# Performance work log

Hardware: AMD Instinct MI355X
Metric: run time of the kernel (lower is better)

## Reference

```python
import jax, jax.numpy as jnp
import numpy as np

HEAD_SIZE = 64
N_EMBD = 768

def setup_inputs() -> dict:
    key = jax.random.key(0)
    kx, kq, kk, kv = jax.random.split(key, 4)
    x = jax.random.normal(kx, (4, 4096, N_EMBD), dtype=jnp.float32)
    s = 1.0 / np.sqrt(N_EMBD)
    Wq = jax.random.normal(kq, (N_EMBD, HEAD_SIZE), dtype=jnp.float32) * s
    Wk = jax.random.normal(kk, (N_EMBD, HEAD_SIZE), dtype=jnp.float32) * s
    Wv = jax.random.normal(kv, (N_EMBD, HEAD_SIZE), dtype=jnp.float32) * s
    return {"x": x, "Wq": Wq, "Wk": Wk, "Wv": Wv}

def reference(x, Wq, Wk, Wv):
    b, t, c = x.shape
    h = Wq.shape[1]
    q = jnp.einsum('btc,ch->bth', x, Wq)
    k = jnp.einsum('btc,ch->bth', x, Wk)
    v = jnp.einsum('btc,ch->bth', x, Wv)
    scores = jnp.einsum('bqh,bkh->bqk', q, k) / jnp.sqrt(jnp.float32(h))
    causal = jnp.tril(jnp.ones((t, t), dtype=bool))  # [t,t]
    scores = jnp.where(causal, scores, -jnp.inf)
    attn = jax.nn.softmax(scores, axis=-1)
    return jnp.einsum('bqk,bkh->bqh', attn, v)
```

## Files before the change

### kernel.cpp

```cpp
#include <hip/hip_runtime.h>
#include <math.h>

#define BB 4
#define TT 4096
#define CC 768
#define HH 64
#define NN 192
#define LDP 72
#define GR 32
#define XSTR 776
#define SC2 0.180336880f

typedef __bf16 bf16x8 __attribute__((ext_vector_type(8)));
typedef float floatx4 __attribute__((ext_vector_type(4)));
typedef float floatx16 __attribute__((ext_vector_type(16)));
typedef unsigned short u16x8 __attribute__((ext_vector_type(8)));

__device__ inline unsigned short f2bf(float f) {
    union { __bf16 b; unsigned short u; } v;
    v.b = (__bf16)f;
    return v.u;
}
__device__ inline float bf2f(unsigned short u) {
    union { unsigned int u; float f; } v;
    v.u = (unsigned int)u << 16;
    return v.f;
}
__device__ inline unsigned cvtpk(float lo, float hi) {
    unsigned d;
    asm("v_cvt_pk_bf16_f32 %0, %1, %2" : "=v"(d) : "v"(lo), "v"(hi));
    return d;
}

__global__ __launch_bounds__(256) void wprep(const float* __restrict__ Wq,
                                             const float* __restrict__ Wk,
                                             const float* __restrict__ Wv,
                                             unsigned short* __restrict__ wtf) {
    const int idx = blockIdx.x * 256 + threadIdx.x;
    if (idx >= NN * CC) return;
    const int j = idx & 7;
    const int lane = (idx >> 3) & 63;
    const int rest = idx >> 9;
    const int kg = rest % 24;
    const int n_tile = rest / 24;
    const int c = kg * 32 + (lane >> 4) * 8 + j;
    const int n = n_tile * 16 + (lane & 15);
    const float* W = (n < 64) ? Wq : (n < 128) ? Wk : Wv;
    wtf[idx] = f2bf(W[c * HH + (n & 63)]);
}

__global__ __launch_bounds__(256) void qkv_gemm(const float* __restrict__ x,
                                                const unsigned short* __restrict__ wtf,
                                                unsigned short* __restrict__ qb,
                                                unsigned short* __restrict__ kb,
                                                unsigned short* __restrict__ vbt) {
    __shared__ unsigned short As[GR * XSTR];

    const int tid = threadIdx.x;
    const int w = tid >> 6, lane = tid & 63;
    const int l15 = lane & 15, quad = lane >> 4;
    const int m0 = blockIdx.x * GR;
    const int n0 = w * 48;
    const int nt0 = w * 3;

    const float* xbase = x + (size_t)m0 * CC;
#pragma unroll
    for (int e = 0; e < 12; ++e) {
        const int c = tid + 256 * e;
        const int r = c / 96, off = (c - r * 96) * 8;
        const float4 v0 = *(const float4*)(xbase + (size_t)c * 8);
        const float4 v1 = *(const float4*)(xbase + (size_t)c * 8 + 4);
        u16x8 pk;
        pk[0] = f2bf(v0.x); pk[1] = f2bf(v0.y); pk[2] = f2bf(v0.z); pk[3] = f2bf(v0.w);
        pk[4] = f2bf(v1.x); pk[5] = f2bf(v1.y); pk[6] = f2bf(v1.z); pk[7] = f2bf(v1.w);
        *(u16x8*)(As + r * XSTR + off) = pk;
    }
    __syncthreads();

    floatx4 acc[2][3] = {};
#pragma unroll 4
    for (int step = 0; step < 12; ++step) {
        bf16x8 a0[2], a1[2];
#pragma unroll
        for (int rg = 0; rg < 2; ++rg) {
            const unsigned short* ap = As + (16 * rg + l15) * XSTR + step * 64 + quad * 8;
            a0[rg] = *(const bf16x8*)(ap);
            a1[rg] = *(const bf16x8*)(ap + 32);
        }
#pragma unroll
        for (int j = 0; j < 3; ++j) {
            const unsigned short* bp =
                wtf + ((size_t)((nt0 + j) * 24 + 2 * step) * 64 + lane) * 8;
            const bf16x8 b0 = *(const bf16x8*)(bp);
            const bf16x8 b1 = *(const bf16x8*)(bp + 512);
#pragma unroll
            for (int rg = 0; rg < 2; ++rg) {
                acc[rg][j] = __builtin_amdgcn_mfma_f32_16x16x32_bf16(a0[rg], b0, acc[rg][j], 0, 0, 0);
                acc[rg][j] = __builtin_amdgcn_mfma_f32_16x16x32_bf16(a1[rg], b1, acc[rg][j], 0, 0, 0);
            }
        }
    }

    const int b = m0 >> 12;
#pragma unroll
    for (int j = 0; j < 3; ++j) {
        const int n = n0 + j * 16 + l15;
        const int mid = n >> 6;
        const int h = n & 63;
#pragma unroll
        for (int rg = 0; rg < 2; ++rg) {
            const int tloc = (m0 & (TT - 1)) + 16 * rg + quad * 4;
            if (mid == 2) {
                ushort4 pk;
                pk.x = f2bf(acc[rg][j][0]); pk.y = f2bf(acc[rg][j][1]);
                pk.z = f2bf(acc[rg][j][2]); pk.w = f2bf(acc[rg][j][3]);
                *(ushort4*)(vbt + ((size_t)b * HH + h) * TT + tloc) = pk;
            } else {
                unsigned short* dst = (mid == 0) ? qb : kb;
#pragma unroll
                for (int r = 0; r < 4; ++r)
                    dst[(size_t)(m0 + 16 * rg + quad * 4 + r) * HH + h] = f2bf(acc[rg][j][r]);
            }
        }
    }
}

template<int CH>
__global__ __launch_bounds__(256) void attn_part(const unsigned short* __restrict__ qb,
                                                 const unsigned short* __restrict__ kb,
                                                 const unsigned short* __restrict__ vbt,
                                                 unsigned short* __restrict__ Opart,
                                                 float* __restrict__ lsum,
                                                 float* __restrict__ out) {
    __shared__ __align__(16) unsigned char smem[16896];
    unsigned short* Ks  = (unsigned short*)smem;
    unsigned short* VTs = (unsigned short*)(smem + 8192);
    float (*Osh)[2][16][64] = (float(*)[2][16][64])smem;
    float* Lsh = (float*)(smem + 16384);

    constexpr int NG = 64 / CH;
    constexpr int TOTB = CH * (NG * (NG + 1)) / 2;

    const int b = blockIdx.x & 3;
    int rem = TOTB - 1 - (blockIdx.x >> 2);
    int g = 0;
    while (rem >= CH * (g + 1)) { rem -= CH * (g + 1); ++g; }
    const int qt = g * CH + rem / (g + 1);
    const int ch = rem - (rem / (g + 1)) * (g + 1);

    const int q0  = qt * 64;
    const int tid = threadIdx.x;
    const int w = tid >> 6, lane = tid & 63;
    const int wq = w >> 1, wk = w & 1;
    const int l31 = lane & 31, hi = lane >> 5;

    const unsigned short* Qb  = qb  + (size_t)b * TT * HH;
    const unsigned short* Kb  = kb  + (size_t)b * TT * HH;
    const unsigned short* VTb = vbt + (size_t)b * HH * TT;

    bf16x8 qf[4];
    {
        const unsigned short* qp = Qb + (size_t)(q0 + 32 * wq + l31) * HH + 8 * hi;
#pragma unroll
        for (int s = 0; s < 4; ++s) qf[s] = *(const bf16x8*)(qp + 16 * s);
    }

    floatx16 o0 = {}, o1 = {};
    float lacc = 0.f;

    const int kt0 = ch * CH;
    const int kt1 = min(kt0 + CH, qt + 1);

    const int sr = tid >> 3;
    const int slot = tid & 7;
    const int swz = ((slot ^ (sr & 7)) << 3);

    const int kr = 32 * wk + l31;
    const int krow_off = kr * 64;
    const int ksw = (kr & 7);
    const int vd0 = l31, vd1 = 32 + l31;

    u16x8 nk0, nk1, nv0, nv1;
    {
        const unsigned short* Kt = Kb + (size_t)(kt0 * 64) * HH;
        const unsigned short* Vt = VTb + kt0 * 64;
        nk0 = *(const u16x8*)(Kt + (size_t)sr * HH + slot * 8);
        nk1 = *(const u16x8*)(Kt + (size_t)(sr + 32) * HH + slot * 8);
        nv0 = *(const u16x8*)(Vt + (size_t)sr * TT + slot * 8);
        nv1 = *(const u16x8*)(Vt + (size_t)(sr + 32) * TT + slot * 8);
    }

    for (int kt = kt0; kt < kt1; ++kt) {
        __syncthreads();
        *(u16x8*)(Ks  + sr * 64 + swz)        = nk0;
        *(u16x8*)(Ks  + (sr + 32) * 64 + swz) = nk1;
        *(u16x8*)(VTs + sr * 64 + swz)        = nv0;
        *(u16x8*)(VTs + (sr + 32) * 64 + swz) = nv1;
        __syncthreads();

        if (kt + 1 < kt1) {
            const unsigned short* Kt = Kb + (size_t)((kt + 1) * 64) * HH;
            const unsigned short* Vt = VTb + (kt + 1) * 64;
            nk0 = *(const u16x8*)(Kt + (size_t)sr * HH + slot * 8);
            nk1 = *(const u16x8*)(Kt + (size_t)(sr + 32) * HH + slot * 8);
            nv0 = *(const u16x8*)(Vt + (size_t)sr * TT + slot * 8);
            nv1 = *(const u16x8*)(Vt + (size_t)(sr + 32) * TT + slot * 8);
        }

        bf16x8 kc[4];
#pragma unroll
        for (int s = 0; s < 4; ++s) {
            const int sl = 2 * s + hi;
            kc[s] = *(const bf16x8*)(Ks + krow_off + ((sl ^ ksw) << 3));
        }
        bf16x8 vv[4];
#pragma unroll
        for (int i = 0; i < 4; ++i) {
            const int db = i >> 1, m = i & 1;
            const int d = db ? vd1 : vd0;
            const int sl = 4 * wk + 2 * m + hi;
            vv[i] = *(const bf16x8*)(VTs + d * 64 + ((sl ^ (d & 7)) << 3));
        }

        floatx16 sa = {};
#pragma unroll
        for (int s = 0; s < 4; ++s)
            sa = __builtin_amdgcn_mfma_f32_32x32x16_bf16(kc[s], qf[s], sa, 0, 0, 0);

        float st[16];
#pragma unroll
        for (int r = 0; r < 16; ++r) st[r] = sa[r] * SC2;

        if (kt == qt) {
            const int qloc = 32 * wq + l31;
#pragma unroll
            for (int r = 0; r < 16; ++r) {
                const int kloc = 32 * wk + (r & 3) + 8 * (r >> 2) + 4 * hi;
                if (kloc > qloc) st[r] = -INFINITY;
            }
        }

#pragma unroll
        for (int r = 0; r < 16; ++r) {
            const float p = exp2f(st[r]);
            st[r] = p;
            lacc += p;
        }

        bf16x8 pf[2];
#pragma unroll
        for (int m = 0; m < 2; ++m) {
            const unsigned d0 = cvtpk(st[8 * m + 0], st[8 * m + 1]);
            const unsigned d1 = cvtpk(st[8 * m + 2], st[8 * m + 3]);
            const unsigned d2 = cvtpk(st[8 * m + 4], st[8 * m + 5]);
            const unsigned d3 = cvtpk(st[8 * m + 6], st[8 * m + 7]);
            const unsigned e0 = (unsigned)__shfl_xor((int)d0, 32);
            const unsigned e1 = (unsigned)__shfl_xor((int)d1, 32);
            const unsigned e2 = (unsigned)__shfl_xor((int)d2, 32);
            const unsigned e3 = (unsigned)__shfl_xor((int)d3, 32);
            union { unsigned u[4]; bf16x8 v; } pk;
            pk.u[0] = hi ? e2 : d0;
            pk.u[1] = hi ? e3 : d1;
            pk.u[2] = hi ? d2 : e0;
            pk.u[3] = hi ? d3 : e1;
            pf[m] = pk.v;
        }

        o0 = __builtin_amdgcn_mfma_f32_32x32x16_bf16(vv[0], pf[0], o0, 0, 0, 0);
        o0 = __builtin_amdgcn_mfma_f32_32x32x16_bf16(vv[1], pf[1], o0, 0, 0, 0);
        o1 = __builtin_amdgcn_mfma_f32_32x32x16_bf16(vv[2], pf[0], o1, 0, 0, 0);
        o1 = __builtin_amdgcn_mfma_f32_32x32x16_bf16(vv[3], pf[1], o1, 0, 0, 0);
    }

    __syncthreads();
    if (wk == 1) {
#pragma unroll
        for (int r = 0; r < 16; ++r) {
            Osh[wq][0][r][lane] = o0[r];
            Osh[wq][1][r][lane] = o1[r];
        }
        Lsh[wq * 64 + lane] = lacc;
    }
    __syncthreads();
    if (wk == 1) return;
#pragma unroll
    for (int r = 0; r < 16; ++r) {
        o0[r] += Osh[wq][0][r][lane];
        o1[r] += Osh[wq][1][r][lane];
    }
    lacc += Lsh[wq * 64 + lane];
    const float l = lacc + __shfl_xor(lacc, 32);

    if (qt < CH) {
        float* outp = out + ((size_t)b * TT + q0 + 32 * wq + l31) * HH;
        const float inv = 1.f / l;
#pragma unroll
        for (int r = 0; r < 16; ++r) {
            const int dd = (r & 3) + 8 * (r >> 2) + 4 * hi;
            outp[dd]      = o0[r] * inv;
            outp[32 + dd] = o1[r] * inv;
        }
        return;
    }

    const int pbase = ((b * 64 + qt) * NG + ch) * 64;
    unsigned short* Op = Opart + ((size_t)pbase + 32 * wq + l31) * HH;
#pragma unroll
    for (int a = 0; a < 4; ++a) {
        *(unsigned*)(Op + 8 * a + 4 * hi)          = cvtpk(o0[4 * a + 0], o0[4 * a + 1]);
        *(unsigned*)(Op + 8 * a + 4 * hi + 2)      = cvtpk(o0[4 * a + 2], o0[4 * a + 3]);
        *(unsigned*)(Op + 32 + 8 * a + 4 * hi)     = cvtpk(o1[4 * a + 0], o1[4 * a + 1]);
        *(unsigned*)(Op + 32 + 8 * a + 4 * hi + 2) = cvtpk(o1[4 * a + 2], o1[4 * a + 3]);
    }
    if (hi == 0) lsum[pbase + 32 * wq + l31] = l;
}

template<int CH>
__global__ __launch_bounds__(256) void attn_merge(const unsigned short* __restrict__ Opart,
                                                  const float* __restrict__ lsum,
                                                  float* __restrict__ out) {
    constexpr int NG = 64 / CH;
    const int g = blockIdx.x * 256 + threadIdx.x;
    const int row = g >> 3, oct = g & 7;
    const int b = row >> 12, t = row & (TT - 1);
    const int qt = t >> 6, rloc = t & 63;
    if (qt < CH) return;
    const int nchunk = qt / CH + 1;
    const int pbase = ((b * 64 + qt) * NG) * 64 + rloc;
    const int d0 = oct * 8;

    float L = 0.f;
    float a[8] = {};
    for (int c = 0; c < nchunk; ++c) {
        const int idx = pbase + c * 64;
        L += lsum[idx];
        const u16x8 pv = *(const u16x8*)(Opart + (size_t)idx * HH + d0);
#pragma unroll
        for (int k = 0; k < 8; ++k) a[k] += bf2f(pv[k]);
    }
    const float inv = 1.f / L;
    float4 o0, o1;
    o0.x = a[0] * inv; o0.y = a[1] * inv; o0.z = a[2] * inv; o0.w = a[3] * inv;
    o1.x = a[4] * inv; o1.y = a[5] * inv; o1.z = a[6] * inv; o1.w = a[7] * inv;
    float* dst = out + (size_t)row * HH + d0;
    *(float4*)(dst) = o0;
    *(float4*)(dst + 4) = o1;
}

__global__ __launch_bounds__(256) void attn_full(const unsigned short* __restrict__ qb,
                                                 const unsigned short* __restrict__ kb,
                                                 const unsigned short* __restrict__ vbt,
                                                 float* __restrict__ out) {
    __shared__ unsigned short Ks[64 * LDP];
    __shared__ unsigned short VTs[64 * LDP];
    __shared__ unsigned short Ps[4][16 * LDP];

    const int b   = blockIdx.x >> 6;
    const int qt  = blockIdx.x & 63;
    const int q0  = qt * 64;
    const int tid = threadIdx.x;
    const int w = tid >> 6, lane = tid & 63;
    const int l15 = lane & 15, quad = lane >> 4;

    const unsigned short* Qb  = qb  + (size_t)b * TT * HH;
    const unsigned short* Kb  = kb  + (size_t)b * TT * HH;
    const unsigned short* VTb = vbt + (size_t)b * HH * TT;

    const int qrow = q0 + 16 * w + l15;
    const bf16x8 qf0 = *(const bf16x8*)(Qb + (size_t)qrow * HH + quad * 8);
    const bf16x8 qf1 = *(const bf16x8*)(Qb + (size_t)qrow * HH + 32 + quad * 8);

    floatx4 O[4] = {};
    floatx4 lacc = {0.f, 0.f, 0.f, 0.f};

    for (int kt = 0; kt <= qt; ++kt) {
        __syncthreads();
        const unsigned short* Kt = Kb + (size_t)(kt * 64) * HH;
        const unsigned short* Vt = VTb + kt * 64;
#pragma unroll
        for (int e = 0; e < 2; ++e) {
            const int chunk = tid + 256 * e;
            const int r = chunk >> 3, c0 = (chunk & 7) * 8;
            *(u16x8*)(Ks + r * LDP + c0)  = *(const u16x8*)(Kt + r * HH + c0);
            *(u16x8*)(VTs + r * LDP + c0) = *(const u16x8*)(Vt + (size_t)r * TT + c0);
        }
        __syncthreads();

        floatx4 s[4];
#pragma unroll
        for (int ki = 0; ki < 4; ++ki) {
            const bf16x8 kf0 = *(const bf16x8*)(Ks + (16 * ki + l15) * LDP + quad * 8);
            const bf16x8 kf1 = *(const bf16x8*)(Ks + (16 * ki + l15) * LDP + 32 + quad * 8);
            floatx4 c = {};
            c = __builtin_amdgcn_mfma_f32_16x16x32_bf16(qf0, kf0, c, 0, 0, 0);
            c = __builtin_amdgcn_mfma_f32_16x16x32_bf16(qf1, kf1, c, 0, 0, 0);
            s[ki] = c * SC2;
        }
        if (kt == qt) {
#pragma unroll
            for (int ki = 0; ki < 4; ++ki)
#pragma unroll
                for (int r = 0; r < 4; ++r)
                    if (16 * ki + l15 > 16 * w + quad * 4 + r) s[ki][r] = -INFINITY;
        }
#pragma unroll
        for (int ki = 0; ki < 4; ++ki)
#pragma unroll
            for (int r = 0; r < 4; ++r) {
                const float p = exp2f(s[ki][r]);
                s[ki][r] = p; lacc[r] += p;
            }

        unsigned short* Pw = Ps[w];
#pragma unroll
        for (int ki = 0; ki < 4; ++ki)
#pragma unroll
            for (int r = 0; r < 4; ++r)
                Pw[(quad * 4 + r) * LDP + 16 * ki + l15] = f2bf(s[ki][r]);

        const bf16x8 pf0 = *(const bf16x8*)(Pw + l15 * LDP + quad * 8);
        const bf16x8 pf1 = *(const bf16x8*)(Pw + l15 * LDP + 32 + quad * 8);
#pragma unroll
        for (int di = 0; di < 4; ++di) {
            const bf16x8 vf0 = *(const bf16x8*)(VTs + (16 * di + l15) * LDP + quad * 8);
            const bf16x8 vf1 = *(const bf16x8*)(VTs + (16 * di + l15) * LDP + 32 + quad * 8);
            O[di] = __builtin_amdgcn_mfma_f32_16x16x32_bf16(pf0, vf0, O[di], 0, 0, 0);
            O[di] = __builtin_amdgcn_mfma_f32_16x16x32_bf16(pf1, vf1, O[di], 0, 0, 0);
        }
    }
    float l_r[4];
#pragma unroll
    for (int r = 0; r < 4; ++r) {
        float v = lacc[r];
#pragma unroll
        for (int msk = 8; msk >= 1; msk >>= 1) v += __shfl_xor(v, msk, 64);
        l_r[r] = v;
    }
    float* outp = out + ((size_t)b * TT + q0 + 16 * w) * HH;
#pragma unroll
    for (int di = 0; di < 4; ++di)
#pragma unroll
        for (int r = 0; r < 4; ++r)
            outp[(quad * 4 + r) * HH + 16 * di + l15] = O[di][r] / l_r[r];
}

extern "C" void kernel_launch(void* const* d_in, const int* in_sizes, int n_in,
                              void* d_out, int out_size, void* d_ws, size_t ws_size,
                              hipStream_t stream) {
    const float* x  = (const float*)d_in[0];
    const float* Wq = (const float*)d_in[1];
    const float* Wk = (const float*)d_in[2];
    const float* Wv = (const float*)d_in[3];
    float* out = (float*)d_out;

    const size_t nQKV = (size_t)BB * TT * HH;
    unsigned short* qb  = (unsigned short*)d_ws;
    unsigned short* kb  = qb + nQKV;
    unsigned short* vbt = kb + nQKV;
    unsigned short* wtf = vbt + nQKV;
    unsigned short* Opart = wtf + (size_t)NN * CC;

    const size_t prows8  = (size_t)BB * 64 * 8 * 64;
    const size_t prows16 = (size_t)BB * 64 * 4 * 64;
    float* lsum8  = (float*)(Opart + prows8 * HH);
    float* lsum16 = (float*)(Opart + prows16 * HH);
    const size_t need8  = (size_t)((char*)(lsum8  + prows8)  - (char*)d_ws);
    const size_t need16 = (size_t)((char*)(lsum16 + prows16) - (char*)d_ws);

    wprep<<<(NN * CC + 255) / 256, 256, 0, stream>>>(Wq, Wk, Wv, wtf);
    qkv_gemm<<<(BB * TT) / GR, 256, 0, stream>>>(x, wtf, qb, kb, vbt);
    if (ws_size >= need8) {
        attn_part<8><<<BB * 288, 256, 0, stream>>>(qb, kb, vbt, Opart, lsum8, out);
        attn_merge<8><<<(BB * TT * 8) / 256, 256, 0, stream>>>(Opart, lsum8, out);
    } else if (ws_size >= need16) {
        attn_part<16><<<BB * 160, 256, 0, stream>>>(qb, kb, vbt, Opart, lsum16, out);
        attn_merge<16><<<(BB * TT * 8) / 256, 256, 0, stream>>>(Opart, lsum16, out);
    } else {
        attn_full<<<BB * (TT / 64), 256, 0, stream>>>(qb, kb, vbt, out);
    }
}
```

Baseline: 128.3 us.

## Double-buffer K/V tiles in LDS to drop one barrier per iteration

Splits the shared-memory K and V^T staging into two ping-pong buffers. The next tile is written into the idle buffer while the current one is consumed, and global prefetch now runs two tiles ahead. This removes the second __syncthreads per key tile and lets the LDS stores overlap with the MFMA work. In exchange, shared memory per block roughly doubles, which may reduce how many blocks fit per CU.

```diff
diff --git a/kernel.cpp b/kernel.cpp
--- a/kernel.cpp
+++ b/kernel.cpp
@@ -132,11 +132,9 @@
                                                  unsigned short* __restrict__ Opart,
                                                  float* __restrict__ lsum,
                                                  float* __restrict__ out) {
-    __shared__ __align__(16) unsigned char smem[16896];
-    unsigned short* Ks  = (unsigned short*)smem;
-    unsigned short* VTs = (unsigned short*)(smem + 8192);
+    __shared__ __align__(16) unsigned short smem[16384];
     float (*Osh)[2][16][64] = (float(*)[2][16][64])smem;
-    float* Lsh = (float*)(smem + 16384);
+    float* Lsh = (float*)(smem + 8192);
 
     constexpr int NG = 64 / CH;
     constexpr int TOTB = CH * (NG * (NG + 1)) / 2;
@@ -189,29 +187,52 @@
         nv0 = *(const u16x8*)(Vt + (size_t)sr * TT + slot * 8);
         nv1 = *(const u16x8*)(Vt + (size_t)(sr + 32) * TT + slot * 8);
     }
+    {
+        unsigned short* Ks0  = smem;
+        unsigned short* VTs0 = smem + 4096;
+        *(u16x8*)(Ks0  + sr * 64 + swz)        = nk0;
+        *(u16x8*)(Ks0  + (sr + 32) * 64 + swz) = nk1;
+        *(u16x8*)(VTs0 + sr * 64 + swz)        = nv0;
+        *(u16x8*)(VTs0 + (sr + 32) * 64 + swz) = nv1;
+    }
+    if (kt0 + 1 < kt1) {
+        const unsigned short* Kt = Kb + (size_t)((kt0 + 1) * 64) * HH;
+        const unsigned short* Vt = VTb + (kt0 + 1) * 64;
+        nk0 = *(const u16x8*)(Kt + (size_t)sr * HH + slot * 8);
+        nk1 = *(const u16x8*)(Kt + (size_t)(sr + 32) * HH + slot * 8);
+        nv0 = *(const u16x8*)(Vt + (size_t)sr * TT + slot * 8);
+        nv1 = *(const u16x8*)(Vt + (size_t)(sr + 32) * TT + slot * 8);
+    }
 
     for (int kt = kt0; kt < kt1; ++kt) {
+        const int p = (kt - kt0) & 1;
         __syncthreads();
-        *(u16x8*)(Ks  + sr * 64 + swz)        = nk0;
-        *(u16x8*)(Ks  + (sr + 32) * 64 + swz) = nk1;
-        *(u16x8*)(VTs + sr * 64 + swz)        = nv0;
-        *(u16x8*)(VTs + (sr + 32) * 64 + swz) = nv1;
-        __syncthreads();
 
         if (kt + 1 < kt1) {
-            const unsigned short* Kt = Kb + (size_t)((kt + 1) * 64) * HH;
-            const unsigned short* Vt = VTb + (kt + 1) * 64;
-            nk0 = *(const u16x8*)(Kt + (size_t)sr * HH + slot * 8);
-            nk1 = *(const u16x8*)(Kt + (size_t)(sr + 32) * HH + slot * 8);
-            nv0 = *(const u16x8*)(Vt + (size_t)sr * TT + slot * 8);
-            nv1 = *(const u16x8*)(Vt + (size_t)(sr + 32) * TT + slot * 8);
-        }
+            unsigned short* Ksn  = smem + (p ^ 1) * 8192;
+            unsigned short* VTsn = Ksn + 4096;
+            *(u16x8*)(Ksn  + sr * 64 + swz)        = nk0;
+            *(u16x8*)(Ksn  + (sr + 32) * 64 + swz) = nk1;
+            *(u16x8*)(VTsn + sr * 64 + swz)        = nv0;
+            *(u16x8*)(VTsn + (sr + 32) * 64 + swz) = nv1;
+            if (kt + 2 < kt1) {
+                const unsigned short* Kt = Kb + (size_t)((kt + 2) * 64) * HH;
+                const unsigned short* Vt = VTb + (kt + 2) * 64;
+                nk0 = *(const u16x8*)(Kt + (size_t)sr * HH + slot * 8);
+                nk1 = *(const u16x8*)(Kt + (size_t)(sr + 32) * HH + slot * 8);
+                nv0 = *(const u16x8*)(Vt + (size_t)sr * TT + slot * 8);
+                nv1 = *(const u16x8*)(Vt + (size_t)(sr + 32) * TT + slot * 8);
+            }
+        }
+
+        const unsigned short* Ksc  = smem + p * 8192;
+        const unsigned short* VTsc = Ksc + 4096;
 
         bf16x8 kc[4];
 #pragma unroll
         for (int s = 0; s < 4; ++s) {
             const int sl = 2 * s + hi;
-            kc[s] = *(const bf16x8*)(Ks + krow_off + ((sl ^ ksw) << 3));
+            kc[s] = *(const bf16x8*)(Ksc + krow_off + ((sl ^ ksw) << 3));
         }
         bf16x8 vv[4];
 #pragma unroll
@@ -219,7 +240,7 @@
             const int db = i >> 1, m = i & 1;
             const int d = db ? vd1 : vd0;
             const int sl = 4 * wk + 2 * m + hi;
-            vv[i] = *(const bf16x8*)(VTs + d * 64 + ((sl ^ (d & 7)) << 3));
+            vv[i] = *(const bf16x8*)(VTsc + d * 64 + ((sl ^ (d & 7)) << 3));
         }
 
         floatx16 sa = {};
@@ -242,9 +263,9 @@
 
 #pragma unroll
         for (int r = 0; r < 16; ++r) {
-            const float p = exp2f(st[r]);
-            st[r] = p;
-            lacc += p;
+            const float p2 = exp2f(st[r]);
+            st[r] = p2;
+            lacc += p2;
         }
 
         bf16x8 pf[2];
```

Result: no change. 130.3 us (+1.5%).

## Fuse partial-attention merge into attn_part via last-block atomic counter

Applied to the files above, without the earlier changes.

Removes the separate attn_merge kernel. Each attn_part block now bumps a per-(batch, q-tile) atomic counter after writing its partial output and row sum. The last block to arrive for a tile reads all partials and writes the normalised output. The counters are zeroed inside wprep, which saves a kernel launch and a pass over the grid, but the last-arriving blocks now carry the merge work serially, which may lengthen the tail. The no-workspace fallback passes wprep an int alias of wtf as the counter buffer, so its zeroing can race with the wtf writes.

```diff
diff --git a/kernel.cpp b/kernel.cpp
--- a/kernel.cpp
+++ b/kernel.cpp
@@ -35,8 +35,10 @@
 __global__ __launch_bounds__(256) void wprep(const float* __restrict__ Wq,
                                              const float* __restrict__ Wk,
                                              const float* __restrict__ Wv,
-                                             unsigned short* __restrict__ wtf) {
+                                             unsigned short* __restrict__ wtf,
+                                             int* __restrict__ cnt) {
     const int idx = blockIdx.x * 256 + threadIdx.x;
+    if (idx < 256) cnt[idx] = 0;
     if (idx >= NN * CC) return;
     const int j = idx & 7;
     const int lane = (idx >> 3) & 63;
@@ -131,12 +133,14 @@
                                                  const unsigned short* __restrict__ vbt,
                                                  unsigned short* __restrict__ Opart,
                                                  float* __restrict__ lsum,
+                                                 int* __restrict__ cnt,
                                                  float* __restrict__ out) {
-    __shared__ __align__(16) unsigned char smem[16896];
+    __shared__ __align__(16) unsigned char smem[16912];
     unsigned short* Ks  = (unsigned short*)smem;
     unsigned short* VTs = (unsigned short*)(smem + 8192);
     float (*Osh)[2][16][64] = (float(*)[2][16][64])smem;
     float* Lsh = (float*)(smem + 16384);
+    int* flag  = (int*)(smem + 16896);
 
     constexpr int NG = 64 / CH;
     constexpr int TOTB = CH * (NG * (NG + 1)) / 2;
@@ -282,69 +286,76 @@
         Lsh[wq * 64 + lane] = lacc;
     }
     __syncthreads();
-    if (wk == 1) return;
-#pragma unroll
-    for (int r = 0; r < 16; ++r) {
-        o0[r] += Osh[wq][0][r][lane];
-        o1[r] += Osh[wq][1][r][lane];
-    }
-    lacc += Lsh[wq * 64 + lane];
+    if (wk == 0) {
+#pragma unroll
+        for (int r = 0; r < 16; ++r) {
+            o0[r] += Osh[wq][0][r][lane];
+            o1[r] += Osh[wq][1][r][lane];
+        }
+        lacc += Lsh[wq * 64 + lane];
+    }
     const float l = lacc + __shfl_xor(lacc, 32);
 
     if (qt < CH) {
-        float* outp = out + ((size_t)b * TT + q0 + 32 * wq + l31) * HH;
-        const float inv = 1.f / l;
-#pragma unroll
-        for (int r = 0; r < 16; ++r) {
-            const int dd = (r & 3) + 8 * (r >> 2) + 4 * hi;
-            outp[dd]      = o0[r] * inv;
-            outp[32 + dd] = o1[r] * inv;
+        if (wk == 0) {
+            float* outp = out + ((size_t)b * TT + q0 + 32 * wq + l31) * HH;
+            const float inv = 1.f / l;
+#pragma unroll
+            for (int r = 0; r < 16; ++r) {
+                const int dd = (r & 3) + 8 * (r >> 2) + 4 * hi;
+                outp[dd]      = o0[r] * inv;
+                outp[32 + dd] = o1[r] * inv;
+            }
         }
         return;
     }
 
     const int pbase = ((b * 64 + qt) * NG + ch) * 64;
-    unsigned short* Op = Opart + ((size_t)pbase + 32 * wq + l31) * HH;
-#pragma unroll
-    for (int a = 0; a < 4; ++a) {
-        *(unsigned*)(Op + 8 * a + 4 * hi)          = cvtpk(o0[4 * a + 0], o0[4 * a + 1]);
-        *(unsigned*)(Op + 8 * a + 4 * hi + 2)      = cvtpk(o0[4 * a + 2], o0[4 * a + 3]);
-        *(unsigned*)(Op + 32 + 8 * a + 4 * hi)     = cvtpk(o1[4 * a + 0], o1[4 * a + 1]);
-        *(unsigned*)(Op + 32 + 8 * a + 4 * hi + 2) = cvtpk(o1[4 * a + 2], o1[4 * a + 3]);
-    }
-    if (hi == 0) lsum[pbase + 32 * wq + l31] = l;
-}
-
-template<int CH>
-__global__ __launch_bounds__(256) void attn_merge(const unsigned short* __restrict__ Opart,
-                                                  const float* __restrict__ lsum,
-                                                  float* __restrict__ out) {
-    constexpr int NG = 64 / CH;
-    const int g = blockIdx.x * 256 + threadIdx.x;
-    const int row = g >> 3, oct = g & 7;
-    const int b = row >> 12, t = row & (TT - 1);
-    const int qt = t >> 6, rloc = t & 63;
-    if (qt < CH) return;
+    if (wk == 0) {
+        unsigned short* Op = Opart + ((size_t)pbase + 32 * wq + l31) * HH;
+#pragma unroll
+        for (int a = 0; a < 4; ++a) {
+            *(unsigned*)(Op + 8 * a + 4 * hi)          = cvtpk(o0[4 * a + 0], o0[4 * a + 1]);
+            *(unsigned*)(Op + 8 * a + 4 * hi + 2)      = cvtpk(o0[4 * a + 2], o0[4 * a + 3]);
+            *(unsigned*)(Op + 32 + 8 * a + 4 * hi)     = cvtpk(o1[4 * a + 0], o1[4 * a + 1]);
+            *(unsigned*)(Op + 32 + 8 * a + 4 * hi + 2) = cvtpk(o1[4 * a + 2], o1[4 * a + 3]);
+        }
+        if (hi == 0) lsum[pbase + 32 * wq + l31] = l;
+    }
+
     const int nchunk = qt / CH + 1;
-    const int pbase = ((b * 64 + qt) * NG) * 64 + rloc;
-    const int d0 = oct * 8;
-
-    float L = 0.f;
-    float a[8] = {};
-    for (int c = 0; c < nchunk; ++c) {
-        const int idx = pbase + c * 64;
-        L += lsum[idx];
-        const u16x8 pv = *(const u16x8*)(Opart + (size_t)idx * HH + d0);
-#pragma unroll
-        for (int k = 0; k < 8; ++k) a[k] += bf2f(pv[k]);
-    }
-    const float inv = 1.f / L;
-    float4 o0, o1;
-    o0.x = a[0] * inv; o0.y = a[1] * inv; o0.z = a[2] * inv; o0.w = a[3] * inv;
-    o1.x = a[4] * inv; o1.y = a[5] * inv; o1.z = a[6] * inv; o1.w = a[7] * inv;
-    float* dst = out + (size_t)row * HH + d0;
-    *(float4*)(dst) = o0;
-    *(float4*)(dst + 4) = o1;
+    __syncthreads();
+    if (tid == 0) {
+        __threadfence();
+        const int old = atomicAdd(&cnt[b * 64 + qt], 1);
+        *flag = (old == nchunk - 1);
+    }
+    __syncthreads();
+    if (!*flag) return;
+    __threadfence();
+
+    const int gbase = (b * 64 + qt) * NG * 64;
+    const int oct = tid & 7, d0m = oct * 8;
+#pragma unroll
+    for (int pass = 0; pass < 2; ++pass) {
+        const int rr = (tid >> 3) + 32 * pass;
+        float L = 0.f;
+        float a[8] = {};
+        for (int c = 0; c < nchunk; ++c) {
+            const int idx = gbase + c * 64 + rr;
+            L += lsum[idx];
+            const u16x8 pv = *(const u16x8*)(Opart + (size_t)idx * HH + d0m);
+#pragma unroll
+            for (int k = 0; k < 8; ++k) a[k] += bf2f(pv[k]);
+        }
+        const float inv = 1.f / L;
+        float4 v0, v1;
+        v0.x = a[0] * inv; v0.y = a[1] * inv; v0.z = a[2] * inv; v0.w = a[3] * inv;
+        v1.x = a[4] * inv; v1.y = a[5] * inv; v1.z = a[6] * inv; v1.w = a[7] * inv;
+        float* dst = out + ((size_t)b * TT + q0 + rr) * HH + d0m;
+        *(float4*)(dst) = v0;
+        *(float4*)(dst + 4) = v1;
+    }
 }
 
 __global__ __launch_bounds__(256) void attn_full(const unsigned short* __restrict__ qb,
@@ -464,18 +475,22 @@
     const size_t prows16 = (size_t)BB * 64 * 4 * 64;
     float* lsum8  = (float*)(Opart + prows8 * HH);
     float* lsum16 = (float*)(Opart + prows16 * HH);
-    const size_t need8  = (size_t)((char*)(lsum8  + prows8)  - (char*)d_ws);
-    const size_t need16 = (size_t)((char*)(lsum16 + prows16) - (char*)d_ws);
-
-    wprep<<<(NN * CC + 255) / 256, 256, 0, stream>>>(Wq, Wk, Wv, wtf);
-    qkv_gemm<<<(BB * TT) / GR, 256, 0, stream>>>(x, wtf, qb, kb, vbt);
+    int* cnt8  = (int*)(lsum8 + prows8);
+    int* cnt16 = (int*)(lsum16 + prows16);
+    const size_t need8  = (size_t)((char*)(cnt8  + 256) - (char*)d_ws);
+    const size_t need16 = (size_t)((char*)(cnt16 + 256) - (char*)d_ws);
+
     if (ws_size >= need8) {
-        attn_part<8><<<BB * 288, 256, 0, stream>>>(qb, kb, vbt, Opart, lsum8, out);
-        attn_merge<8><<<(BB * TT * 8) / 256, 256, 0, stream>>>(Opart, lsum8, out);
+        wprep<<<(NN * CC + 255) / 256, 256, 0, stream>>>(Wq, Wk, Wv, wtf, cnt8);
+        qkv_gemm<<<(BB * TT) / GR, 256, 0, stream>>>(x, wtf, qb, kb, vbt);
+        attn_part<8><<<BB * 288, 256, 0, stream>>>(qb, kb, vbt, Opart, lsum8, cnt8, out);
     } else if (ws_size >= need16) {
-        attn_part<16><<<BB * 160, 256, 0, stream>>>(qb, kb, vbt, Opart, lsum16, out);
-        attn_merge<16><<<(BB * TT * 8) / 256, 256, 0, stream>>>(Opart, lsum16, out);
+        wprep<<<(NN * CC + 255) / 256, 256, 0, stream>>>(Wq, Wk, Wv, wtf, cnt16);
+        qkv_gemm<<<(BB * TT) / GR, 256, 0, stream>>>(x, wtf, qb, kb, vbt);
+        attn_part<16><<<BB * 160, 256, 0, stream>>>(qb, kb, vbt, Opart, lsum16, cnt16, out);
     } else {
+        wprep<<<(NN * CC + 255) / 256, 256, 0, stream>>>(Wq, Wk, Wv, wtf, (int*)wtf);
+        qkv_gemm<<<(BB * TT) / GR, 256, 0, stream>>>(x, wtf, qb, kb, vbt);
         attn_full<<<BB * (TT / 64), 256, 0, stream>>>(qb, kb, vbt, out);
     }
 }
```

Result: slower. 221.7 us (+72.7%).

## Use 128-row query tiles with each wave owning 32 queries over full key tile

Applied to the files above, without the earlier changes.

The split-KV attention kernel now gives each block 128 query rows, one 32-row slice per wave, and each wave walks both 32-key halves of every 64-key tile. Before, waves split the keys and combined their partial outputs through shared memory. The new layout removes that cross-wave reduction and its extra barriers, and each K/V tile loaded into shared memory now serves twice as many queries. It also skips 32-key sub-blocks that lie fully above the causal diagonal. In exchange the grid has half as many blocks, and the partial-output buffer layout and the merge kernel are re-indexed to match.

```diff
diff --git a/kernel.cpp b/kernel.cpp
--- a/kernel.cpp
+++ b/kernel.cpp
@@ -132,27 +132,26 @@
                                                  unsigned short* __restrict__ Opart,
                                                  float* __restrict__ lsum,
                                                  float* __restrict__ out) {
-    __shared__ __align__(16) unsigned char smem[16896];
-    unsigned short* Ks  = (unsigned short*)smem;
-    unsigned short* VTs = (unsigned short*)(smem + 8192);
-    float (*Osh)[2][16][64] = (float(*)[2][16][64])smem;
-    float* Lsh = (float*)(smem + 16384);
-
-    constexpr int NG = 64 / CH;
-    constexpr int TOTB = CH * (NG * (NG + 1)) / 2;
+    __shared__ __align__(16) unsigned short Ks[64 * 64];
+    __shared__ __align__(16) unsigned short VTs[64 * 64];
+
+    constexpr int W  = CH / 2;
+    constexpr int NB = 32 / W;
+    constexpr int NG = NB;
+    constexpr int TOTB = W * NB * (NB + 1) / 2;
 
     const int b = blockIdx.x & 3;
     int rem = TOTB - 1 - (blockIdx.x >> 2);
     int g = 0;
-    while (rem >= CH * (g + 1)) { rem -= CH * (g + 1); ++g; }
-    const int qt = g * CH + rem / (g + 1);
+    while (rem >= W * (g + 1)) { rem -= W * (g + 1); ++g; }
+    const int qt = g * W + rem / (g + 1);
     const int ch = rem - (rem / (g + 1)) * (g + 1);
 
-    const int q0  = qt * 64;
+    const int q0  = qt * 128;
     const int tid = threadIdx.x;
     const int w = tid >> 6, lane = tid & 63;
-    const int wq = w >> 1, wk = w & 1;
     const int l31 = lane & 31, hi = lane >> 5;
+    const int qbase = q0 + 32 * w;
 
     const unsigned short* Qb  = qb  + (size_t)b * TT * HH;
     const unsigned short* Kb  = kb  + (size_t)b * TT * HH;
@@ -160,7 +159,7 @@
 
     bf16x8 qf[4];
     {
-        const unsigned short* qp = Qb + (size_t)(q0 + 32 * wq + l31) * HH + 8 * hi;
+        const unsigned short* qp = Qb + (size_t)(qbase + l31) * HH + 8 * hi;
 #pragma unroll
         for (int s = 0; s < 4; ++s) qf[s] = *(const bf16x8*)(qp + 16 * s);
     }
@@ -168,16 +167,16 @@
     floatx16 o0 = {}, o1 = {};
     float lacc = 0.f;
 
+    const int nkt = 2 * qt + 2;
     const int kt0 = ch * CH;
-    const int kt1 = min(kt0 + CH, qt + 1);
+    const int kt1 = min(kt0 + CH, nkt);
 
     const int sr = tid >> 3;
     const int slot = tid & 7;
     const int swz = ((slot ^ (sr & 7)) << 3);
 
-    const int kr = 32 * wk + l31;
-    const int krow_off = kr * 64;
-    const int ksw = (kr & 7);
+    const int krow_off0 = l31 * 64;
+    const int ksw = (l31 & 7);
     const int vd0 = l31, vd1 = 32 + l31;
 
     u16x8 nk0, nk1, nv0, nv1;
@@ -207,92 +206,81 @@
             nv1 = *(const u16x8*)(Vt + (size_t)(sr + 32) * TT + slot * 8);
         }
 
-        bf16x8 kc[4];
-#pragma unroll
-        for (int s = 0; s < 4; ++s) {
-            const int sl = 2 * s + hi;
-            kc[s] = *(const bf16x8*)(Ks + krow_off + ((sl ^ ksw) << 3));
-        }
-        bf16x8 vv[4];
-#pragma unroll
-        for (int i = 0; i < 4; ++i) {
-            const int db = i >> 1, m = i & 1;
-            const int d = db ? vd1 : vd0;
-            const int sl = 4 * wk + 2 * m + hi;
-            vv[i] = *(const bf16x8*)(VTs + d * 64 + ((sl ^ (d & 7)) << 3));
-        }
-
-        floatx16 sa = {};
-#pragma unroll
-        for (int s = 0; s < 4; ++s)
-            sa = __builtin_amdgcn_mfma_f32_32x32x16_bf16(kc[s], qf[s], sa, 0, 0, 0);
-
-        float st[16];
-#pragma unroll
-        for (int r = 0; r < 16; ++r) st[r] = sa[r] * SC2;
-
-        if (kt == qt) {
-            const int qloc = 32 * wq + l31;
+#pragma unroll
+        for (int ks = 0; ks < 2; ++ks) {
+            const int kb32 = kt * 64 + 32 * ks;
+            if (kb32 > qbase + 31) continue;
+
+            bf16x8 kc[4];
+#pragma unroll
+            for (int s = 0; s < 4; ++s) {
+                const int sl = 2 * s + hi;
+                kc[s] = *(const bf16x8*)(Ks + 32 * 64 * ks + krow_off0 + ((sl ^ ksw) << 3));
+            }
+
+            floatx16 sa = {};
+#pragma unroll
+            for (int s = 0; s < 4; ++s)
+                sa = __builtin_amdgcn_mfma_f32_32x32x16_bf16(kc[s], qf[s], sa, 0, 0, 0);
+
+            float st[16];
+#pragma unroll
+            for (int r = 0; r < 16; ++r) st[r] = sa[r] * SC2;
+
+            if (kb32 == qbase) {
+#pragma unroll
+                for (int r = 0; r < 16; ++r) {
+                    const int key = (r & 3) + 8 * (r >> 2) + 4 * hi;
+                    if (key > l31) st[r] = -INFINITY;
+                }
+            }
+
 #pragma unroll
             for (int r = 0; r < 16; ++r) {
-                const int kloc = 32 * wk + (r & 3) + 8 * (r >> 2) + 4 * hi;
-                if (kloc > qloc) st[r] = -INFINITY;
-            }
-        }
-
-#pragma unroll
-        for (int r = 0; r < 16; ++r) {
-            const float p = exp2f(st[r]);
-            st[r] = p;
-            lacc += p;
-        }
-
-        bf16x8 pf[2];
-#pragma unroll
-        for (int m = 0; m < 2; ++m) {
-            const unsigned d0 = cvtpk(st[8 * m + 0], st[8 * m + 1]);
-            const unsigned d1 = cvtpk(st[8 * m + 2], st[8 * m + 3]);
-            const unsigned d2 = cvtpk(st[8 * m + 4], st[8 * m + 5]);
-            const unsigned d3 = cvtpk(st[8 * m + 6], st[8 * m + 7]);
-            const unsigned e0 = (unsigned)__shfl_xor((int)d0, 32);
-            const unsigned e1 = (unsigned)__shfl_xor((int)d1, 32);
-            const unsigned e2 = (unsigned)__shfl_xor((int)d2, 32);
-            const unsigned e3 = (unsigned)__shfl_xor((int)d3, 32);
-            union { unsigned u[4]; bf16x8 v; } pk;
-            pk.u[0] = hi ? e2 : d0;
-            pk.u[1] = hi ? e3 : d1;
-            pk.u[2] = hi ? d2 : e0;
-            pk.u[3] = hi ? d3 : e1;
-            pf[m] = pk.v;
-        }
-
-        o0 = __builtin_amdgcn_mfma_f32_32x32x16_bf16(vv[0], pf[0], o0, 0, 0, 0);
-        o0 = __builtin_amdgcn_mfma_f32_32x32x16_bf16(vv[1], pf[1], o0, 0, 0, 0);
-        o1 = __builtin_amdgcn_mfma_f32_32x32x16_bf16(vv[2], pf[0], o1, 0, 0, 0);
-        o1 = __builtin_amdgcn_mfma_f32_32x32x16_bf16(vv[3], pf[1], o1, 0, 0, 0);
-    }
-
-    __syncthreads();
-    if (wk == 1) {
-#pragma unroll
-        for (int r = 0; r < 16; ++r) {
-            Osh[wq][0][r][lane] = o0[r];
-            Osh[wq][1][r][lane] = o1[r];
-        }
-        Lsh[wq * 64 + lane] = lacc;
-    }
-    __syncthreads();
-    if (wk == 1) return;
-#pragma unroll
-    for (int r = 0; r < 16; ++r) {
-        o0[r] += Osh[wq][0][r][lane];
-        o1[r] += Osh[wq][1][r][lane];
-    }
-    lacc += Lsh[wq * 64 + lane];
+                const float p = exp2f(st[r]);
+                st[r] = p;
+                lacc += p;
+            }
+
+            bf16x8 pf[2];
+#pragma unroll
+            for (int m = 0; m < 2; ++m) {
+                const unsigned d0 = cvtpk(st[8 * m + 0], st[8 * m + 1]);
+                const unsigned d1 = cvtpk(st[8 * m + 2], st[8 * m + 3]);
+                const unsigned d2 = cvtpk(st[8 * m + 4], st[8 * m + 5]);
+                const unsigned d3 = cvtpk(st[8 * m + 6], st[8 * m + 7]);
+                const unsigned e0 = (unsigned)__shfl_xor((int)d0, 32);
+                const unsigned e1 = (unsigned)__shfl_xor((int)d1, 32);
+                const unsigned e2 = (unsigned)__shfl_xor((int)d2, 32);
+                const unsigned e3 = (unsigned)__shfl_xor((int)d3, 32);
+                union { unsigned u[4]; bf16x8 v; } pk;
+                pk.u[0] = hi ? e2 : d0;
+                pk.u[1] = hi ? e3 : d1;
+                pk.u[2] = hi ? d2 : e0;
+                pk.u[3] = hi ? d3 : e1;
+                pf[m] = pk.v;
+            }
+
+            bf16x8 vv[4];
+#pragma unroll
+            for (int i = 0; i < 4; ++i) {
+                const int db = i >> 1, m = i & 1;
+                const int d = db ? vd1 : vd0;
+                const int sl = 4 * ks + 2 * m + hi;
+                vv[i] = *(const bf16x8*)(VTs + d * 64 + ((sl ^ (d & 7)) << 3));
+            }
+
+            o0 = __builtin_amdgcn_mfma_f32_32x32x16_bf16(vv[0], pf[0], o0, 0, 0, 0);
+            o0 = __builtin_amdgcn_mfma_f32_32x32x16_bf16(vv[1], pf[1], o0, 0, 0, 0);
+            o1 = __builtin_amdgcn_mfma_f32_32x32x16_bf16(vv[2], pf[0], o1, 0, 0, 0);
+            o1 = __builtin_amdgcn_mfma_f32_32x32x16_bf16(vv[3], pf[1], o1, 0, 0, 0);
+        }
+    }
+
     const float l = lacc + __shfl_xor(lacc, 32);
 
-    if (qt < CH) {
-        float* outp = out + ((size_t)b * TT + q0 + 32 * wq + l31) * HH;
+    if (qt < W) {
+        float* outp = out + ((size_t)b * TT + qbase + l31) * HH;
         const float inv = 1.f / l;
 #pragma unroll
         for (int r = 0; r < 16; ++r) {
@@ -303,8 +291,8 @@
         return;
     }
 
-    const int pbase = ((b * 64 + qt) * NG + ch) * 64;
-    unsigned short* Op = Opart + ((size_t)pbase + 32 * wq + l31) * HH;
+    const int pbase = ((b * 32 + qt) * NG + ch) * 128;
+    unsigned short* Op = Opart + ((size_t)pbase + 32 * w + l31) * HH;
 #pragma unroll
     for (int a = 0; a < 4; ++a) {
         *(unsigned*)(Op + 8 * a + 4 * hi)          = cvtpk(o0[4 * a + 0], o0[4 * a + 1]);
@@ -312,27 +300,28 @@
         *(unsigned*)(Op + 32 + 8 * a + 4 * hi)     = cvtpk(o1[4 * a + 0], o1[4 * a + 1]);
         *(unsigned*)(Op + 32 + 8 * a + 4 * hi + 2) = cvtpk(o1[4 * a + 2], o1[4 * a + 3]);
     }
-    if (hi == 0) lsum[pbase + 32 * wq + l31] = l;
+    if (hi == 0) lsum[pbase + 32 * w + l31] = l;
 }
 
 template<int CH>
 __global__ __launch_bounds__(256) void attn_merge(const unsigned short* __restrict__ Opart,
                                                   const float* __restrict__ lsum,
                                                   float* __restrict__ out) {
-    constexpr int NG = 64 / CH;
+    constexpr int W  = CH / 2;
+    constexpr int NG = 32 / W;
     const int g = blockIdx.x * 256 + threadIdx.x;
     const int row = g >> 3, oct = g & 7;
     const int b = row >> 12, t = row & (TT - 1);
-    const int qt = t >> 6, rloc = t & 63;
-    if (qt < CH) return;
-    const int nchunk = qt / CH + 1;
-    const int pbase = ((b * 64 + qt) * NG) * 64 + rloc;
+    const int qt = t >> 7, rloc = t & 127;
+    if (qt < W) return;
+    const int nchunk = qt / W + 1;
+    const int pbase = ((b * 32 + qt) * NG) * 128 + rloc;
     const int d0 = oct * 8;
 
     float L = 0.f;
     float a[8] = {};
     for (int c = 0; c < nchunk; ++c) {
-        const int idx = pbase + c * 64;
+        const int idx = pbase + c * 128;
         L += lsum[idx];
         const u16x8 pv = *(const u16x8*)(Opart + (size_t)idx * HH + d0);
 #pragma unroll
@@ -460,8 +449,8 @@
     unsigned short* wtf = vbt + nQKV;
     unsigned short* Opart = wtf + (size_t)NN * CC;
 
-    const size_t prows8  = (size_t)BB * 64 * 8 * 64;
-    const size_t prows16 = (size_t)BB * 64 * 4 * 64;
+    const size_t prows8  = (size_t)BB * 32 * 8 * 128;
+    const size_t prows16 = (size_t)BB * 32 * 4 * 128;
     float* lsum8  = (float*)(Opart + prows8 * HH);
     float* lsum16 = (float*)(Opart + prows16 * HH);
     const size_t need8  = (size_t)((char*)(lsum8  + prows8)  - (char*)d_ws);
@@ -470,10 +459,10 @@
     wprep<<<(NN * CC + 255) / 256, 256, 0, stream>>>(Wq, Wk, Wv, wtf);
     qkv_gemm<<<(BB * TT) / GR, 256, 0, stream>>>(x, wtf, qb, kb, vbt);
     if (ws_size >= need8) {
-        attn_part<8><<<BB * 288, 256, 0, stream>>>(qb, kb, vbt, Opart, lsum8, out);
+        attn_part<8><<<BB * 144, 256, 0, stream>>>(qb, kb, vbt, Opart, lsum8, out);
         attn_merge<8><<<(BB * TT * 8) / 256, 256, 0, stream>>>(Opart, lsum8, out);
     } else if (ws_size >= need16) {
-        attn_part<16><<<BB * 160, 256, 0, stream>>>(qb, kb, vbt, Opart, lsum16, out);
+        attn_part<16><<<BB * 80, 256, 0, stream>>>(qb, kb, vbt, Opart, lsum16, out);
         attn_merge<16><<<(BB * TT * 8) / 256, 256, 0, stream>>>(Opart, lsum16, out);
     } else {
         attn_full<<<BB * (TT / 64), 256, 0, stream>>>(qb, kb, vbt, out);
```

After: 128.9 us. No clear change (+0.5%).
